# Kernel tuning notes

Hardware: AMD Instinct MI355X
Metric: run time of the kernel (lower is better)

## Reference

```python
import jax, jax.numpy as jnp
import numpy as np
from jax import lax

C = 512   # n_feat == Cn == Cdim (forced by DA_conv/CA_layer consistency)
H, W = 16, 32  # reshape_codebooks(512)
K = 3     # kernel_size
RED = 8   # reduction


def _lrelu(x):
    return jax.nn.leaky_relu(x, 0.1)


def _conv1x1(x, w, b=None):
    # x: (B,C,H,W), w: (O,C) -- torch Conv2d(.,.,1) weight squeezed
    y = jnp.einsum('oc,bchw->bohw', w, x)
    if b is not None:
        y = y + b[None, :, None, None]
    return y


def _conv3x3(x, w, b):
    # x: (B,C,H,W), w: (O,C,3,3) OIHW, padding=k//2 == SAME for odd k
    y = lax.conv_general_dilated(x, w, (1, 1), 'SAME',
                                 dimension_numbers=('NCHW', 'OIHW', 'NCHW'))
    return y + b[None, :, None, None]


def _da_conv(c, deg, kw1, kw2, pw, pb, caw1, caw2):
    # per-channel dynamic kernels from degradation vectors: (Cn, K*K)
    kern = (_lrelu(deg @ kw1.T) @ kw2.T).reshape(C, 1, K, K)
    # depthwise conv, groups = b1*c1 = C (b1 == 1)
    out = lax.conv_general_dilated(c, kern, (1, 1), 'SAME',
                                   feature_group_count=C,
                                   dimension_numbers=('NCHW', 'OIHW', 'NCHW'))
    out = _lrelu(out)
    out = _conv1x1(out, pw, pb)
    # CA_layer: deg reshaped to (1, Cn, 16, 32), channel attention, deg * att
    dr = deg.reshape(1, C, H, W)
    att = jax.nn.sigmoid(_conv1x1(_lrelu(_conv1x1(dr, caw1)), caw2))
    return out + dr * att


def setup_inputs() -> dict:
    key = jax.random.key(0)
    ks = jax.random.split(key, 16)
    n = lambda i, shape, s=0.05: jax.random.normal(ks[i], shape, dtype=jnp.float32) * s
    return dict(
        c=jax.random.normal(ks[0], (1, C, H, W), dtype=jnp.float32),
        deg=jax.random.normal(ks[1], (C, C), dtype=jnp.float32) * 0.1,
        k1_w1=n(2, (C, C)), k1_w2=n(3, (K * K, C)),
        p1_w=n(4, (C, C)), p1_b=jnp.zeros((C,), jnp.float32),
        ca1_w1=n(5, (C // RED, C)), ca1_w2=n(6, (C, C // RED)),
        conv1_w=n(7, (C, C, K, K)), conv1_b=jnp.zeros((C,), jnp.float32),
        k2_w1=n(8, (C, C)), k2_w2=n(9, (K * K, C)),
        p2_w=n(10, (C, C)), p2_b=jnp.zeros((C,), jnp.float32),
        ca2_w1=n(11, (C // RED, C)), ca2_w2=n(12, (C, C // RED)),
        conv2_w=n(13, (C, C, K, K)), conv2_b=jnp.zeros((C,), jnp.float32),
    )


def reference(c, deg, k1_w1, k1_w2, p1_w, p1_b, ca1_w1, ca1_w2,
              conv1_w, conv1_b, k2_w1, k2_w2, p2_w, p2_b,
              ca2_w1, ca2_w2, conv2_w, conv2_b):
    out = _lrelu(_da_conv(c, deg, k1_w1, k1_w2, p1_w, p1_b, ca1_w1, ca1_w2))
    out = _lrelu(_conv3x3(out, conv1_w, conv1_b))
    out = _lrelu(_da_conv(out, deg, k2_w1, k2_w2, p2_w, p2_b, ca2_w1, ca2_w2))
    return _conv3x3(out, conv2_w, conv2_b) + c
```

## Files before the change

### kernel.cpp

```cpp
#include <hip/hip_runtime.h>
#include <hip/hip_bf16.h>

typedef __attribute__((ext_vector_type(8))) unsigned short ushort8;
typedef __attribute__((ext_vector_type(8))) __bf16 bf16x8;
typedef __attribute__((ext_vector_type(4))) float f32x4;
typedef __attribute__((ext_vector_type(4))) unsigned short ushort4v;

__device__ __forceinline__ float lrelu_f(float v){ return v > 0.f ? v : 0.1f*v; }

__device__ __forceinline__ unsigned short f2bf(float v){
  unsigned u = __float_as_uint(v);
  unsigned r = (u + 0x7fffu + ((u>>16)&1u)) >> 16;
  return (unsigned short)r;
}

__device__ __forceinline__ void packq(const float* __restrict__ s,
                                      unsigned short* __restrict__ d, int i){
  const float4 v = ((const float4*)s)[i];
  ushort4v o; o.x=f2bf(v.x); o.y=f2bf(v.y); o.z=f2bf(v.z); o.w=f2bf(v.w);
  *(ushort4v*)(d + (size_t)i*4) = o;
}

__global__ __launch_bounds__(256) void k_pack_all(
  const float* __restrict__ k1_w1, const float* __restrict__ k2_w1,
  const float* __restrict__ p1_w,  const float* __restrict__ p2_w,
  const float* __restrict__ ca1_w1,const float* __restrict__ ca1_w2,
  const float* __restrict__ ca2_w1,const float* __restrict__ ca2_w2,
  const float* __restrict__ deg,   const float* __restrict__ conv1_w,
  const float* __restrict__ conv2_w,
  unsigned short* __restrict__ K1B, unsigned short* __restrict__ K2B,
  unsigned short* __restrict__ P1B, unsigned short* __restrict__ P2B,
  unsigned short* __restrict__ CA1A,unsigned short* __restrict__ CA1B,
  unsigned short* __restrict__ CA2A,unsigned short* __restrict__ CA2B,
  unsigned short* __restrict__ DEGB,unsigned short* __restrict__ DEGT,
  unsigned short* __restrict__ WB1, unsigned short* __restrict__ WB2){
  int i = blockIdx.x*256 + threadIdx.x;
  if (i < 65536){ packq(k1_w1, K1B, i); return; } i -= 65536;
  if (i < 65536){ packq(k2_w1, K2B, i); return; } i -= 65536;
  if (i < 65536){ packq(p1_w,  P1B, i); return; } i -= 65536;
  if (i < 65536){ packq(p2_w,  P2B, i); return; } i -= 65536;
  if (i < 8192){ packq(ca1_w1, CA1A, i); return; } i -= 8192;
  if (i < 8192){ packq(ca1_w2, CA1B, i); return; } i -= 8192;
  if (i < 8192){ packq(ca2_w1, CA2A, i); return; } i -= 8192;
  if (i < 8192){ packq(ca2_w2, CA2B, i); return; } i -= 8192;
  if (i < 65536){ packq(deg, DEGB, i); return; } i -= 65536;
  if (i < 65536){
    const int j = i*4; const int p = j>>9, c = j&511;
    ushort4v o;
    o.x = f2bf(deg[(size_t)(c+0)*512 + p]);
    o.y = f2bf(deg[(size_t)(c+1)*512 + p]);
    o.z = f2bf(deg[(size_t)(c+2)*512 + p]);
    o.w = f2bf(deg[(size_t)(c+3)*512 + p]);
    *(ushort4v*)(DEGT + (size_t)j) = o;
    return;
  } i -= 65536;
  if (i < 589824){
    const int o_ = i/1152; const int r4 = (i - o_*1152)*4;
    const int t = r4>>9; const int ci = r4&511;
    const float* s = conv1_w + (size_t)o_*4608;
    ushort4v o;
    o.x = f2bf(s[(ci+0)*9 + t]); o.y = f2bf(s[(ci+1)*9 + t]);
    o.z = f2bf(s[(ci+2)*9 + t]); o.w = f2bf(s[(ci+3)*9 + t]);
    *(ushort4v*)(WB1 + (size_t)o_*4608 + r4) = o;
    return;
  } i -= 589824;
  if (i < 589824){
    const int o_ = i/1152; const int r4 = (i - o_*1152)*4;
    const int t = r4>>9; const int ci = r4&511;
    const float* s = conv2_w + (size_t)o_*4608;
    ushort4v o;
    o.x = f2bf(s[(ci+0)*9 + t]); o.y = f2bf(s[(ci+1)*9 + t]);
    o.z = f2bf(s[(ci+2)*9 + t]); o.w = f2bf(s[(ci+3)*9 + t]);
    *(ushort4v*)(WB2 + (size_t)o_*4608 + r4) = o;
  }
}

__device__ __forceinline__ void gemm64(
    const unsigned short* __restrict__ A, const unsigned short* __restrict__ Bt,
    int m0, int n0, int K, int tid,
    unsigned short* lA, unsigned short* lB, f32x4 acc[2][2]){
  const int wid = tid>>6, lane = tid&63;
  const int srow = tid>>2, skb = tid&3;
  const unsigned short* gA = A  + (size_t)(m0+srow)*K + skb*8;
  const unsigned short* gB = Bt + (size_t)(n0+srow)*K + skb*8;
  const int soff = srow*32 + 8*(skb ^ (srow&3));
  const int wr = (wid>>1)*32, wc = (wid&1)*32;
  const int l15 = lane&15, lkb = lane>>4;
  int aoff[2], boff[2];
  #pragma unroll
  for (int s=0;s<2;s++){
    const int Ra = wr + s*16 + l15;
    aoff[s] = Ra*32 + 8*(lkb ^ (Ra&3));
    const int Rb = wc + s*16 + l15;
    boff[s] = Rb*32 + 8*(lkb ^ (Rb&3));
  }
  const int nst = K>>5;
  ushort8 ra = *(const ushort8*)gA;
  ushort8 rb = *(const ushort8*)gB;
  for (int st=0; st<nst; ++st){
    ushort8 ra2 = {}, rb2 = {};
    if (st+1 < nst){
      ra2 = *(const ushort8*)(gA+32);
      rb2 = *(const ushort8*)(gB+32);
    }
    gA += 32; gB += 32;
    __syncthreads();
    *(ushort8*)(lA + soff) = ra;
    *(ushort8*)(lB + soff) = rb;
    __syncthreads();
    bf16x8 af[2], bfr[2];
    #pragma unroll
    for (int s=0;s<2;s++){
      af[s]  = *(const bf16x8*)(lA + aoff[s]);
      bfr[s] = *(const bf16x8*)(lB + boff[s]);
    }
    #pragma unroll
    for (int mi=0;mi<2;mi++)
      #pragma unroll
      for (int ni=0;ni<2;ni++)
        acc[mi][ni] = __builtin_amdgcn_mfma_f32_16x16x32_bf16(af[mi], bfr[ni], acc[mi][ni], 0,0,0);
    ra = ra2; rb = rb2;
  }
}

__global__ __launch_bounds__(256) void k_mgemm_pre(
    const unsigned short* __restrict__ DEGB, const unsigned short* __restrict__ DEGT,
    const unsigned short* __restrict__ K1B,  const unsigned short* __restrict__ K2B,
    const unsigned short* __restrict__ CA1A, const unsigned short* __restrict__ CA2A,
    float* __restrict__ TMP1, float* __restrict__ TMP2,
    unsigned short* __restrict__ HID1, unsigned short* __restrict__ HID2){
  const int z = blockIdx.z;
  if (z >= 2 && blockIdx.y != 0) return;
  const unsigned short* A  = (z < 2) ? DEGB : DEGT;
  const unsigned short* Bt = (z==0) ? K1B : (z==1) ? K2B : (z==2) ? CA1A : CA2A;
  __shared__ unsigned short lA[2048], lB[2048];
  const int tid = threadIdx.x;
  const int m0 = blockIdx.x*64, n0 = blockIdx.y*64;
  f32x4 acc[2][2] = {};
  gemm64(A, Bt, m0, n0, 512, tid, lA, lB, acc);

  const int wid = tid>>6, lane = tid&63;
  const int wr = (wid>>1)*32, wc = (wid&1)*32;
  const int l15 = lane&15, lkb = lane>>4;
  #pragma unroll
  for (int mi=0;mi<2;mi++)
    #pragma unroll
    for (int ni=0;ni<2;ni++){
      const int row = m0 + wr + mi*16 + lkb*4;
      const int col = n0 + wc + ni*16 + l15;
      #pragma unroll
      for (int r=0;r<4;r++){
        const float v = lrelu_f(acc[mi][ni][r]);
        if (z==0)      TMP1[(size_t)(row+r)*512 + col] = v;
        else if (z==1) TMP2[(size_t)(row+r)*512 + col] = v;
        else if (z==2) HID1[(size_t)(row+r)*64 + col] = f2bf(v);
        else           HID2[(size_t)(row+r)*64 + col] = f2bf(v);
      }
    }
}

__global__ __launch_bounds__(256) void k_kern_att(
    const float* __restrict__ TMP1, const float* __restrict__ TMP2,
    const float* __restrict__ kw2a, const float* __restrict__ kw2b,
    const unsigned short* __restrict__ CA1B, const unsigned short* __restrict__ CA2B,
    const unsigned short* __restrict__ HID1, const unsigned short* __restrict__ HID2,
    float* __restrict__ kern0, float* __restrict__ kern1,
    float* __restrict__ ATT1, float* __restrict__ ATT2){
  const int z = blockIdx.z;
  const int tid = threadIdx.x;
  if (z < 2){
    const float* tmp  = z ? TMP2 : TMP1;
    const float* kw2  = z ? kw2b : kw2a;
    float* kern       = z ? kern1 : kern0;
    const int i = blockIdx.x*4 + (tid>>6);
    const int lane = tid&63;
    float acc[9];
    #pragma unroll
    for (int q=0;q<9;q++) acc[q]=0.f;
    for (int j=lane; j<512; j+=64){
      const float t = tmp[i*512 + j];
      #pragma unroll
      for (int q=0;q<9;q++) acc[q] += t*kw2[q*512 + j];
    }
    #pragma unroll
    for (int q=0;q<9;q++){
      float v = acc[q];
      #pragma unroll
      for (int off=32; off>0; off>>=1) v += __shfl_down(v, off);
      if (lane==0) kern[i*9+q] = v;
    }
  } else {
    if (blockIdx.x >= 64) return;
    const unsigned short* A  = (z==2) ? CA1B : CA2B;
    const unsigned short* Bt = (z==2) ? HID1 : HID2;
    float* ATT               = (z==2) ? ATT1 : ATT2;
    __shared__ unsigned short lA[2048], lB[2048];
    const int m0 = (blockIdx.x>>3)*64, n0 = (blockIdx.x&7)*64;
    f32x4 acc[2][2] = {};
    gemm64(A, Bt, m0, n0, 64, tid, lA, lB, acc);
    const int wid = tid>>6, lane = tid&63;
    const int wr = (wid>>1)*32, wc = (wid&1)*32;
    const int l15 = lane&15, lkb = lane>>4;
    #pragma unroll
    for (int mi=0;mi<2;mi++)
      #pragma unroll
      for (int ni=0;ni<2;ni++){
        const int row = m0 + wr + mi*16 + lkb*4;
        const int col = n0 + wc + ni*16 + l15;
        #pragma unroll
        for (int r=0;r<4;r++)
          ATT[(size_t)(row+r)*512 + col] = 1.f/(1.f + expf(-acc[mi][ni][r]));
      }
  }
}

__global__ __launch_bounds__(512) void k_dwconv(const float* __restrict__ x,
    const float* __restrict__ kern, unsigned short* __restrict__ yt){
  const int c = blockIdx.x;
  const int p = threadIdx.x;
  const int iy = p>>5, ix = p&31;
  __shared__ float plane[18*34];
  for (int i=p;i<18*34;i+=512) plane[i]=0.f;
  __syncthreads();
  plane[(iy+1)*34 + ix+1] = x[c*512 + p];
  __syncthreads();
  const float* kp = kern + c*9;
  float s = 0.f;
  #pragma unroll
  for (int dy=0;dy<3;dy++)
    #pragma unroll
    for (int dx=0;dx<3;dx++)
      s += plane[(iy+dy)*34 + ix+dx]*kp[dy*3+dx];
  yt[(size_t)p*512 + c] = f2bf(lrelu_f(s));
}

__global__ __launch_bounds__(512) void k_dwconv_red(const float* __restrict__ part,
    const float* __restrict__ bias, const float* __restrict__ kern,
    unsigned short* __restrict__ yt, int nchunks){
  const int c = blockIdx.x;
  const int p = threadIdx.x;
  const int iy = p>>5, ix = p&31;
  __shared__ float plane[18*34];
  for (int i=p;i<18*34;i+=512) plane[i]=0.f;
  float v = bias[c];
  for (int s=0;s<nchunks;s++) v += part[(size_t)s*262144 + c*512 + p];
  v = lrelu_f(v);
  __syncthreads();
  plane[(iy+1)*34 + ix+1] = v;
  __syncthreads();
  const float* kp = kern + c*9;
  float s = 0.f;
  #pragma unroll
  for (int dy=0;dy<3;dy++)
    #pragma unroll
    for (int dx=0;dx<3;dx++)
      s += plane[(iy+dy)*34 + ix+dx]*kp[dy*3+dx];
  yt[(size_t)p*512 + c] = f2bf(lrelu_f(s));
}

__global__ __launch_bounds__(256) void k_pw(
    const unsigned short* __restrict__ A, const unsigned short* __restrict__ Bt,
    const float* __restrict__ bias,
    const float* __restrict__ E1, const float* __restrict__ E2,
    unsigned short* __restrict__ XT){
  __shared__ unsigned short lA[1024], lB[1024];
  __shared__ float tile[32][33];
  const int tid = threadIdx.x;
  const int wid = tid>>6, lane = tid&63;
  const int M0 = blockIdx.x*32, N0 = blockIdx.y*32;

  const int half = tid>>7;
  const int st_ = tid&127;
  const int srow = st_>>2, skb = st_&3;
  const unsigned short* gS = (half ? Bt + (size_t)(N0+srow)*512
                                   : A  + (size_t)(M0+srow)*512) + skb*8;
  unsigned short* lS = (half ? lB : lA);
  const int soff = srow*32 + 8*(skb ^ (srow&3));

  const int wr = (wid>>1)*16, wc = (wid&1)*16;
  const int l15 = lane&15, lkb = lane>>4;
  const int Ra = wr + l15, Rb = wc + l15;
  const int aoff = Ra*32 + 8*(lkb ^ (Ra&3));
  const int boff = Rb*32 + 8*(lkb ^ (Rb&3));

  f32x4 acc = {};
  ushort8 r0 = *(const ushort8*)gS;
  #pragma unroll 1
  for (int st=0; st<16; ++st){
    ushort8 r1 = {};
    if (st < 15) r1 = *(const ushort8*)(gS+32);
    gS += 32;
    __syncthreads();
    *(ushort8*)(lS + soff) = r0;
    __syncthreads();
    const bf16x8 af = *(const bf16x8*)(lA + aoff);
    const bf16x8 bf = *(const bf16x8*)(lB + boff);
    acc = __builtin_amdgcn_mfma_f32_16x16x32_bf16(af, bf, acc, 0,0,0);
    r0 = r1;
  }

  #pragma unroll
  for (int r=0;r<4;r++){
    const int rl = wr + lkb*4 + r;
    const int cl = wc + l15;
    const int rr = M0 + rl, col = N0 + cl;
    float v = acc[r] + bias[rr] + E1[(size_t)rr*512+col]*E2[(size_t)rr*512+col];
    tile[rl][cl] = lrelu_f(v);
  }
  __syncthreads();
  const int pr = tid>>3, q = tid&7;
  ushort4v o;
  o.x = f2bf(tile[q*4+0][pr]); o.y = f2bf(tile[q*4+1][pr]);
  o.z = f2bf(tile[q*4+2][pr]); o.w = f2bf(tile[q*4+3][pr]);
  *(ushort4v*)(XT + (size_t)(N0+pr)*512 + M0 + q*4) = o;
}

template<int KCH>
__global__ __launch_bounds__(256) void k_mfma_conv(
    const unsigned short* __restrict__ WB,
    const unsigned short* __restrict__ XT,
    float* __restrict__ part){
  __shared__ unsigned short lA[2048], lB[2048];
  const int tid = threadIdx.x;
  const int wid = tid>>6, lane = tid&63;
  const int m0 = blockIdx.x*64, n0 = blockIdx.y*64;
  const int k0 = blockIdx.z*KCH;

  const int srow = tid>>2, skb = tid&3;
  const unsigned short* gA = WB + (size_t)(m0+srow)*4608 + k0 + skb*8;
  const int p = n0 + srow, py = p>>5, px = p&31;
  const int soff = srow*32 + 8*(skb ^ (srow&3));

  const int wr = (wid>>1)*32, wc = (wid&1)*32;
  const int l15 = lane&15, lkb = lane>>4;
  int aoff[2], boff[2];
  #pragma unroll
  for (int s=0;s<2;s++){
    const int Ra = wr + s*16 + l15;
    aoff[s] = Ra*32 + 8*(lkb ^ (Ra&3));
    const int Rb = wc + s*16 + l15;
    boff[s] = Rb*32 + 8*(lkb ^ (Rb&3));
  }

  auto loadB = [&](int step)->ushort8 {
    const int k = k0 + step*32;
    const int t = k>>9;
    const int dy = t/3, dx = t - dy*3;
    const int yy = py + dy - 1, xx = px + dx - 1;
    ushort8 r = {};
    if ((unsigned)yy < 16u && (unsigned)xx < 32u)
      r = *(const ushort8*)(XT + (size_t)(yy*32+xx)*512 + (k&511) + skb*8);
    return r;
  };

  constexpr int NST = KCH/32;
  f32x4 acc[2][2] = {};
  ushort8 ra = *(const ushort8*)gA;
  ushort8 rb = loadB(0);
  #pragma unroll 1
  for (int st=0; st<NST; ++st){
    ushort8 ra2 = {}, rb2 = {};
    if (st+1 < NST){
      ra2 = *(const ushort8*)(gA+32);
      rb2 = loadB(st+1);
    }
    gA += 32;
    __syncthreads();
    *(ushort8*)(lA + soff) = ra;
    *(ushort8*)(lB + soff) = rb;
    __syncthreads();
    bf16x8 af[2], bfr[2];
    #pragma unroll
    for (int s=0;s<2;s++){
      af[s]  = *(const bf16x8*)(lA + aoff[s]);
      bfr[s] = *(const bf16x8*)(lB + boff[s]);
    }
    #pragma unroll
    for (int mi=0;mi<2;mi++)
      #pragma unroll
      for (int ni=0;ni<2;ni++)
        acc[mi][ni] = __builtin_amdgcn_mfma_f32_16x16x32_bf16(af[mi], bfr[ni], acc[mi][ni], 0,0,0);
    ra = ra2; rb = rb2;
  }

  float* pbase = part + (size_t)blockIdx.z*262144;
  #pragma unroll
  for (int mi=0;mi<2;mi++)
    #pragma unroll
    for (int ni=0;ni<2;ni++){
      const int row = m0 + wr + mi*16 + lkb*4;
      const int col = n0 + wc + ni*16 + l15;
      #pragma unroll
      for (int r=0;r<4;r++)
        pbase[(size_t)(row+r)*512 + col] = acc[mi][ni][r];
    }
}

__global__ __launch_bounds__(256) void k_reduce_final(const float* __restrict__ part,
    const float* __restrict__ bias, const float* __restrict__ res,
    float* __restrict__ y, int nchunks){
  const int idx = blockIdx.x*256 + threadIdx.x;
  const int o = idx>>9;
  float v = bias[o];
  for (int s=0;s<nchunks;s++) v += part[(size_t)s*262144 + idx];
  y[idx] = v + res[idx];
}

extern "C" void kernel_launch(void* const* d_in, const int* in_sizes, int n_in,
                              void* d_out, int out_size, void* d_ws, size_t ws_size,
                              hipStream_t stream) {
  (void)in_sizes; (void)n_in; (void)out_size;
  const float* xin    = (const float*)d_in[0];
  const float* deg    = (const float*)d_in[1];
  const float* k1_w1  = (const float*)d_in[2];
  const float* k1_w2  = (const float*)d_in[3];
  const float* p1_w   = (const float*)d_in[4];
  const float* p1_b   = (const float*)d_in[5];
  const float* ca1_w1 = (const float*)d_in[6];
  const float* ca1_w2 = (const float*)d_in[7];
  const float* conv1_w= (const float*)d_in[8];
  const float* conv1_b= (const float*)d_in[9];
  const float* k2_w1  = (const float*)d_in[10];
  const float* k2_w2  = (const float*)d_in[11];
  const float* p2_w   = (const float*)d_in[12];
  const float* p2_b   = (const float*)d_in[13];
  const float* ca2_w1 = (const float*)d_in[14];
  const float* ca2_w2 = (const float*)d_in[15];
  const float* conv2_w= (const float*)d_in[16];
  const float* conv2_b= (const float*)d_in[17];
  float* out = (float*)d_out;

  const bool big = ws_size >= (size_t)8202000*4;
  const int NS = big ? 16 : 8;

  float* ws = (float*)d_ws;
  float* PART = ws;  ws += (size_t)NS*262144;
  float* TMP1 = PART;
  float* TMP2 = PART + 262144;
  unsigned short* HID1 = (unsigned short*)(PART + 524288);
  unsigned short* HID2 = HID1 + 32768;
  float* KERN1 = ws;  ws += 4608;
  float* KERN2 = ws;  ws += 4608;
  float* ATT1  = ws;  ws += 262144;
  float* ATT2  = ws;  ws += 262144;
  unsigned short* DEGB = (unsigned short*)ws; ws += 131072;
  unsigned short* DEGT = (unsigned short*)ws; ws += 131072;
  unsigned short* K1B  = (unsigned short*)ws; ws += 131072;
  unsigned short* K2B  = (unsigned short*)ws; ws += 131072;
  unsigned short* P1B  = (unsigned short*)ws; ws += 131072;
  unsigned short* P2B  = (unsigned short*)ws; ws += 131072;
  unsigned short* CA1A = (unsigned short*)ws; ws += 16384;
  unsigned short* CA1B = (unsigned short*)ws; ws += 16384;
  unsigned short* CA2A = (unsigned short*)ws; ws += 16384;
  unsigned short* CA2B = (unsigned short*)ws; ws += 16384;
  unsigned short* DWLT = (unsigned short*)ws; ws += 131072;
  unsigned short* XT   = (unsigned short*)ws; ws += 131072;
  unsigned short* WB1  = (unsigned short*)ws; ws += 1179648;
  unsigned short* WB2  = (unsigned short*)ws; ws += 1179648;

  k_pack_all<<<6272,256,0,stream>>>(k1_w1,k2_w1,p1_w,p2_w,
      ca1_w1,ca1_w2,ca2_w1,ca2_w2, deg, conv1_w, conv2_w,
      K1B,K2B,P1B,P2B, CA1A,CA1B,CA2A,CA2B, DEGB,DEGT, WB1,WB2);

  k_mgemm_pre<<<dim3(8,8,4),256,0,stream>>>(DEGB,DEGT, K1B,K2B, CA1A,CA2A,
      TMP1,TMP2, HID1,HID2);
  k_kern_att<<<dim3(128,1,4),256,0,stream>>>(TMP1,TMP2, k1_w2,k2_w2,
      CA1B,CA2B, HID1,HID2, KERN1,KERN2, ATT1,ATT2);

  k_dwconv<<<512,512,0,stream>>>(xin, KERN1, DWLT);
  k_pw<<<dim3(16,16),256,0,stream>>>(P1B, DWLT, p1_b, deg, ATT1, XT);
  if (big) k_mfma_conv<288><<<dim3(8,8,16),256,0,stream>>>(WB1, XT, PART);
  else     k_mfma_conv<576><<<dim3(8,8,8), 256,0,stream>>>(WB1, XT, PART);
  k_dwconv_red<<<512,512,0,stream>>>(PART, conv1_b, KERN2, DWLT, NS);
  k_pw<<<dim3(16,16),256,0,stream>>>(P2B, DWLT, p2_b, deg, ATT2, XT);
  if (big) k_mfma_conv<288><<<dim3(8,8,16),256,0,stream>>>(WB2, XT, PART);
  else     k_mfma_conv<576><<<dim3(8,8,8), 256,0,stream>>>(WB2, XT, PART);
  k_reduce_final<<<1024,256,0,stream>>>(PART, conv2_b, xin, out, NS);
}
```

Measured before the change: 93.33 us.

## Double-buffer LDS in GEMM loops, widen conv N-tile, vectorize reductions

Converts the gemm64, k_pw and k_mfma_conv main loops to double-buffered shared memory with one barrier per K step, so global loads and LDS writes for the next step overlap MFMA work on the current one. k_mfma_conv now computes a 64x128 tile per block (4 B subtiles per wave), which halves the grid and gives more reuse of each A tile. The split-K reductions in k_dwconv_red and k_reduce_final switch to float4 loads with fewer active threads. The cost is more LDS per block and more registers, which may lower occupancy, and the smaller conv grid may leave compute units idle.

Result: faster. 87.92 us (-5.8%).

```diff
diff --git a/kernel.cpp b/kernel.cpp
--- a/kernel.cpp
+++ b/kernel.cpp
@@ -97,29 +97,33 @@
   const int nst = K>>5;
   ushort8 ra = *(const ushort8*)gA;
   ushort8 rb = *(const ushort8*)gB;
+  *(ushort8*)(lA + soff) = ra;
+  *(ushort8*)(lB + soff) = rb;
+  if (nst > 1){ ra = *(const ushort8*)(gA+32); rb = *(const ushort8*)(gB+32); }
+  __syncthreads();
   for (int st=0; st<nst; ++st){
-    ushort8 ra2 = {}, rb2 = {};
+    const int cur = (st&1)*2048;
+    bf16x8 af[2], bfr[2];
+    #pragma unroll
+    for (int s=0;s<2;s++){
+      af[s]  = *(const bf16x8*)(lA + cur + aoff[s]);
+      bfr[s] = *(const bf16x8*)(lB + cur + boff[s]);
+    }
     if (st+1 < nst){
-      ra2 = *(const ushort8*)(gA+32);
-      rb2 = *(const ushort8*)(gB+32);
-    }
-    gA += 32; gB += 32;
-    __syncthreads();
-    *(ushort8*)(lA + soff) = ra;
-    *(ushort8*)(lB + soff) = rb;
-    __syncthreads();
-    bf16x8 af[2], bfr[2];
-    #pragma unroll
-    for (int s=0;s<2;s++){
-      af[s]  = *(const bf16x8*)(lA + aoff[s]);
-      bfr[s] = *(const bf16x8*)(lB + boff[s]);
+      const int nxt = ((st+1)&1)*2048;
+      *(ushort8*)(lA + nxt + soff) = ra;
+      *(ushort8*)(lB + nxt + soff) = rb;
+      if (st+2 < nst){
+        ra = *(const ushort8*)(gA + (size_t)(st+2)*32);
+        rb = *(const ushort8*)(gB + (size_t)(st+2)*32);
+      }
     }
     #pragma unroll
     for (int mi=0;mi<2;mi++)
       #pragma unroll
       for (int ni=0;ni<2;ni++)
         acc[mi][ni] = __builtin_amdgcn_mfma_f32_16x16x32_bf16(af[mi], bfr[ni], acc[mi][ni], 0,0,0);
-    ra = ra2; rb = rb2;
+    __syncthreads();
   }
 }
 
@@ -133,7 +137,7 @@
   if (z >= 2 && blockIdx.y != 0) return;
   const unsigned short* A  = (z < 2) ? DEGB : DEGT;
   const unsigned short* Bt = (z==0) ? K1B : (z==1) ? K2B : (z==2) ? CA1A : CA2A;
-  __shared__ unsigned short lA[2048], lB[2048];
+  __shared__ unsigned short lA[4096], lB[4096];
   const int tid = threadIdx.x;
   const int m0 = blockIdx.x*64, n0 = blockIdx.y*64;
   f32x4 acc[2][2] = {};
@@ -194,7 +198,7 @@
     const unsigned short* A  = (z==2) ? CA1B : CA2B;
     const unsigned short* Bt = (z==2) ? HID1 : HID2;
     float* ATT               = (z==2) ? ATT1 : ATT2;
-    __shared__ unsigned short lA[2048], lB[2048];
+    __shared__ unsigned short lA[4096], lB[4096];
     const int m0 = (blockIdx.x>>3)*64, n0 = (blockIdx.x&7)*64;
     f32x4 acc[2][2] = {};
     gemm64(A, Bt, m0, n0, 64, tid, lA, lB, acc);
@@ -242,11 +246,20 @@
   const int iy = p>>5, ix = p&31;
   __shared__ float plane[18*34];
   for (int i=p;i<18*34;i+=512) plane[i]=0.f;
-  float v = bias[c];
-  for (int s=0;s<nchunks;s++) v += part[(size_t)s*262144 + c*512 + p];
-  v = lrelu_f(v);
-  __syncthreads();
-  plane[(iy+1)*34 + ix+1] = v;
+  __syncthreads();
+  if (p < 128){
+    const float b = bias[c];
+    float4 a4 = {b,b,b,b};
+    for (int s=0;s<nchunks;s++){
+      const float4 v = ((const float4*)(part + (size_t)s*262144 + c*512))[p];
+      a4.x += v.x; a4.y += v.y; a4.z += v.z; a4.w += v.w;
+    }
+    a4.x = lrelu_f(a4.x); a4.y = lrelu_f(a4.y);
+    a4.z = lrelu_f(a4.z); a4.w = lrelu_f(a4.w);
+    const int px0 = p*4;
+    float* dst = &plane[((px0>>5)+1)*34 + (px0&31)+1];
+    dst[0]=a4.x; dst[1]=a4.y; dst[2]=a4.z; dst[3]=a4.w;
+  }
   __syncthreads();
   const float* kp = kern + c*9;
   float s = 0.f;
@@ -263,7 +276,7 @@
     const float* __restrict__ bias,
     const float* __restrict__ E1, const float* __restrict__ E2,
     unsigned short* __restrict__ XT){
-  __shared__ unsigned short lA[1024], lB[1024];
+  __shared__ unsigned short lA[2][1024], lB[2][1024];
   __shared__ float tile[32][33];
   const int tid = threadIdx.x;
   const int wid = tid>>6, lane = tid&63;
@@ -274,7 +287,7 @@
   const int srow = st_>>2, skb = st_&3;
   const unsigned short* gS = (half ? Bt + (size_t)(N0+srow)*512
                                    : A  + (size_t)(M0+srow)*512) + skb*8;
-  unsigned short* lS = (half ? lB : lA);
+  unsigned short (*lS)[1024] = half ? lB : lA;
   const int soff = srow*32 + 8*(skb ^ (srow&3));
 
   const int wr = (wid>>1)*16, wc = (wid&1)*16;
@@ -285,18 +298,19 @@
 
   f32x4 acc = {};
   ushort8 r0 = *(const ushort8*)gS;
-  #pragma unroll 1
+  *(ushort8*)(&lS[0][soff]) = r0;
+  r0 = *(const ushort8*)(gS+32);
+  __syncthreads();
   for (int st=0; st<16; ++st){
-    ushort8 r1 = {};
-    if (st < 15) r1 = *(const ushort8*)(gS+32);
-    gS += 32;
+    const int cur = st&1;
+    const bf16x8 af = *(const bf16x8*)(&lA[cur][aoff]);
+    const bf16x8 bf = *(const bf16x8*)(&lB[cur][boff]);
+    if (st+1 < 16){
+      *(ushort8*)(&lS[cur^1][soff]) = r0;
+      if (st+2 < 16) r0 = *(const ushort8*)(gS + (size_t)(st+2)*32);
+    }
+    acc = __builtin_amdgcn_mfma_f32_16x16x32_bf16(af, bf, acc, 0,0,0);
     __syncthreads();
-    *(ushort8*)(lS + soff) = r0;
-    __syncthreads();
-    const bf16x8 af = *(const bf16x8*)(lA + aoff);
-    const bf16x8 bf = *(const bf16x8*)(lB + boff);
-    acc = __builtin_amdgcn_mfma_f32_16x16x32_bf16(af, bf, acc, 0,0,0);
-    r0 = r1;
   }
 
   #pragma unroll
@@ -320,30 +334,37 @@
     const unsigned short* __restrict__ WB,
     const unsigned short* __restrict__ XT,
     float* __restrict__ part){
-  __shared__ unsigned short lA[2048], lB[2048];
+  __shared__ unsigned short lA[2][2048], lB[2][4096];
   const int tid = threadIdx.x;
   const int wid = tid>>6, lane = tid&63;
-  const int m0 = blockIdx.x*64, n0 = blockIdx.y*64;
+  const int m0 = blockIdx.x*64, n0 = blockIdx.y*128;
   const int k0 = blockIdx.z*KCH;
 
   const int srow = tid>>2, skb = tid&3;
   const unsigned short* gA = WB + (size_t)(m0+srow)*4608 + k0 + skb*8;
-  const int p = n0 + srow, py = p>>5, px = p&31;
-  const int soff = srow*32 + 8*(skb ^ (srow&3));
-
-  const int wr = (wid>>1)*32, wc = (wid&1)*32;
+  const int soffA = srow*32 + 8*(skb ^ (srow&3));
+  const int brow1 = srow + 64;
+  const int p0 = n0 + srow, p1 = n0 + brow1;
+  const int py0 = p0>>5, px0 = p0&31, py1 = p1>>5, px1 = p1&31;
+  const int soffB0 = srow*32 + 8*(skb ^ (srow&3));
+  const int soffB1 = brow1*32 + 8*(skb ^ (brow1&3));
+
+  const int wr = (wid>>1)*32, wc = (wid&1)*64;
   const int l15 = lane&15, lkb = lane>>4;
-  int aoff[2], boff[2];
+  int aoff[2], boff[4];
   #pragma unroll
   for (int s=0;s<2;s++){
     const int Ra = wr + s*16 + l15;
     aoff[s] = Ra*32 + 8*(lkb ^ (Ra&3));
-    const int Rb = wc + s*16 + l15;
-    boff[s] = Rb*32 + 8*(lkb ^ (Rb&3));
-  }
-
-  auto loadB = [&](int step)->ushort8 {
-    const int k = k0 + step*32;
+  }
+  #pragma unroll
+  for (int u=0;u<4;u++){
+    const int Rb = wc + u*16 + l15;
+    boff[u] = Rb*32 + 8*(lkb ^ (Rb&3));
+  }
+
+  auto ldB = [&](int st, int py, int px)->ushort8 {
+    const int k = k0 + st*32;
     const int t = k>>9;
     const int dy = t/3, dx = t - dy*3;
     const int yy = py + dy - 1, xx = px + dx - 1;
@@ -354,56 +375,72 @@
   };
 
   constexpr int NST = KCH/32;
-  f32x4 acc[2][2] = {};
-  ushort8 ra = *(const ushort8*)gA;
-  ushort8 rb = loadB(0);
-  #pragma unroll 1
+  f32x4 acc[2][4] = {};
+  ushort8 ra  = *(const ushort8*)gA;
+  ushort8 rb0 = ldB(0, py0, px0);
+  ushort8 rb1 = ldB(0, py1, px1);
+  *(ushort8*)(&lA[0][soffA])  = ra;
+  *(ushort8*)(&lB[0][soffB0]) = rb0;
+  *(ushort8*)(&lB[0][soffB1]) = rb1;
+  if (NST > 1){
+    ra  = *(const ushort8*)(gA+32);
+    rb0 = ldB(1, py0, px0);
+    rb1 = ldB(1, py1, px1);
+  }
+  __syncthreads();
   for (int st=0; st<NST; ++st){
-    ushort8 ra2 = {}, rb2 = {};
+    const int cur = st&1;
+    bf16x8 af[2], bfr[4];
+    #pragma unroll
+    for (int s=0;s<2;s++) af[s] = *(const bf16x8*)(&lA[cur][aoff[s]]);
+    #pragma unroll
+    for (int u=0;u<4;u++) bfr[u] = *(const bf16x8*)(&lB[cur][boff[u]]);
     if (st+1 < NST){
-      ra2 = *(const ushort8*)(gA+32);
-      rb2 = loadB(st+1);
-    }
-    gA += 32;
+      const int nxt = cur^1;
+      *(ushort8*)(&lA[nxt][soffA])  = ra;
+      *(ushort8*)(&lB[nxt][soffB0]) = rb0;
+      *(ushort8*)(&lB[nxt][soffB1]) = rb1;
+      if (st+2 < NST){
+        ra  = *(const ushort8*)(gA + (size_t)(st+2)*32);
+        rb0 = ldB(st+2, py0, px0);
+        rb1 = ldB(st+2, py1, px1);
+      }
+    }
+    #pragma unroll
+    for (int s=0;s<2;s++)
+      #pragma unroll
+      for (int u=0;u<4;u++)
+        acc[s][u] = __builtin_amdgcn_mfma_f32_16x16x32_bf16(af[s], bfr[u], acc[s][u], 0,0,0);
     __syncthreads();
-    *(ushort8*)(lA + soff) = ra;
-    *(ushort8*)(lB + soff) = rb;
-    __syncthreads();
-    bf16x8 af[2], bfr[2];
-    #pragma unroll
-    for (int s=0;s<2;s++){
-      af[s]  = *(const bf16x8*)(lA + aoff[s]);
-      bfr[s] = *(const bf16x8*)(lB + boff[s]);
-    }
-    #pragma unroll
-    for (int mi=0;mi<2;mi++)
-      #pragma unroll
-      for (int ni=0;ni<2;ni++)
-        acc[mi][ni] = __builtin_amdgcn_mfma_f32_16x16x32_bf16(af[mi], bfr[ni], acc[mi][ni], 0,0,0);
-    ra = ra2; rb = rb2;
   }
 
   float* pbase = part + (size_t)blockIdx.z*262144;
   #pragma unroll
-  for (int mi=0;mi<2;mi++)
-    #pragma unroll
-    for (int ni=0;ni<2;ni++){
-      const int row = m0 + wr + mi*16 + lkb*4;
-      const int col = n0 + wc + ni*16 + l15;
+  for (int s=0;s<2;s++)
+    #pragma unroll
+    for (int u=0;u<4;u++){
+      const int row = m0 + wr + s*16 + lkb*4;
+      const int col = n0 + wc + u*16 + l15;
       #pragma unroll
       for (int r=0;r<4;r++)
-        pbase[(size_t)(row+r)*512 + col] = acc[mi][ni][r];
+        pbase[(size_t)(row+r)*512 + col] = acc[s][u][r];
     }
 }
 
 __global__ __launch_bounds__(256) void k_reduce_final(const float* __restrict__ part,
     const float* __restrict__ bias, const float* __restrict__ res,
     float* __restrict__ y, int nchunks){
-  const int idx = blockIdx.x*256 + threadIdx.x;
-  const int o = idx>>9;
-  float v = bias[o];
-  for (int s=0;s<nchunks;s++) v += part[(size_t)s*262144 + idx];
-  y[idx] = v + res[idx];
+  const int i = blockIdx.x*256 + threadIdx.x;
+  const int o = i>>7;
+  const float b = bias[o];
+  float4 a4 = {b,b,b,b};
+  for (int s=0;s<nchunks;s++){
+    const float4 v = ((const float4*)part)[(size_t)s*65536 + i];
+    a4.x += v.x; a4.y += v.y; a4.z += v.z; a4.w += v.w;
+  }
+  const float4 rv = ((const float4*)res)[i];
+  a4.x += rv.x; a4.y += rv.y; a4.z += rv.z; a4.w += rv.w;
+  ((float4*)y)[i] = a4;
 }
 
 extern "C" void kernel_launch(void* const* d_in, const int* in_sizes, int n_in,
@@ -469,11 +506,11 @@
 
   k_dwconv<<<512,512,0,stream>>>(xin, KERN1, DWLT);
   k_pw<<<dim3(16,16),256,0,stream>>>(P1B, DWLT, p1_b, deg, ATT1, XT);
-  if (big) k_mfma_conv<288><<<dim3(8,8,16),256,0,stream>>>(WB1, XT, PART);
-  else     k_mfma_conv<576><<<dim3(8,8,8), 256,0,stream>>>(WB1, XT, PART);
+  if (big) k_mfma_conv<288><<<dim3(8,4,16),256,0,stream>>>(WB1, XT, PART);
+  else     k_mfma_conv<576><<<dim3(8,4,8), 256,0,stream>>>(WB1, XT, PART);
   k_dwconv_red<<<512,512,0,stream>>>(PART, conv1_b, KERN2, DWLT, NS);
   k_pw<<<dim3(16,16),256,0,stream>>>(P2B, DWLT, p2_b, deg, ATT2, XT);
-  if (big) k_mfma_conv<288><<<dim3(8,8,16),256,0,stream>>>(WB2, XT, PART);
-  else     k_mfma_conv<576><<<dim3(8,8,8), 256,0,stream>>>(WB2, XT, PART);
-  k_reduce_final<<<1024,256,0,stream>>>(PART, conv2_b, xin, out, NS);
-}
+  if (big) k_mfma_conv<288><<<dim3(8,4,16),256,0,stream>>>(WB2, XT, PART);
+  else     k_mfma_conv<576><<<dim3(8,4,8), 256,0,stream>>>(WB2, XT, PART);
+  k_reduce_final<<<256,256,0,stream>>>(PART, conv2_b, xin, out, NS);
+}
```
